# Kernel tuning notes

Hardware: AMD Instinct MI355X
Metric: run time of the kernel (lower is better)

The kernel has to match this reference:

```python
import jax, jax.numpy as jnp
import numpy as np

N = 50000        # nodes
E = 800000       # edges (before self-loops)
F_IN = 256       # n_features
HID = 32         # hidden_dims (per-head out channels)
HEADS = 4
HC = HID * HEADS # 128, per-layer width
CLASSES = 40
LAYERS = 2
SLOPE = 0.1      # negative_slope for leaky_relu in attention


def _glorot(key, shape):
    fan_in, fan_out = shape[-2], shape[-1]
    lim = np.sqrt(6.0 / (fan_in + fan_out))
    return jax.random.uniform(key, shape, jnp.float32, -lim, lim)


def setup_inputs() -> dict:
    key = jax.random.key(0)
    ks = jax.random.split(key, 7)
    x = jax.random.normal(ks[0], (N, F_IN), jnp.float32)
    edge_index = jax.random.randint(ks[1], (2, E), 0, N, jnp.int64)
    weight_in = _glorot(ks[2], (F_IN, HC))
    weight_out = _glorot(ks[3], (HC, CLASSES))
    Ws = _glorot(ks[4], (LAYERS, HC, HC))            # per-layer GATConv linear
    atts = _glorot(ks[5], (LAYERS, HEADS, 2 * HID))  # [a_src | a_dst] per head
    biases = jnp.zeros((LAYERS, HC), jnp.float32)
    return {"x": x, "edge_index": edge_index, "weight_in": weight_in,
            "Ws": Ws, "atts": atts, "biases": biases, "weight_out": weight_out}


def _gat_conv(h, src, dst, W, att, bias):
    # h: [N, HC]; src/dst: [E'] edge endpoints (message src -> dst)
    n = h.shape[0]
    hp = (h @ W).reshape(n, HEADS, HID)                       # [N, H, C]
    a_src, a_dst = att[:, :HID], att[:, HID:]                 # [H, C] each
    alpha_src = jnp.einsum('nhc,hc->nh', hp, a_src)           # [N, H]
    alpha_dst = jnp.einsum('nhc,hc->nh', hp, a_dst)
    logits = jax.nn.leaky_relu(alpha_src[src] + alpha_dst[dst], SLOPE)  # [E', H]
    # softmax over edges grouped by destination node
    m = jax.ops.segment_max(logits, dst, num_segments=n)      # [N, H]
    e = jnp.exp(logits - m[dst])
    z = jax.ops.segment_sum(e, dst, num_segments=n)           # [N, H]
    alpha = e / z[dst]                                        # [E', H]
    msg = hp[src] * alpha[:, :, None]                         # [E', H, C]
    out = jax.ops.segment_sum(msg, dst, num_segments=n)       # [N, H, C]
    return out.reshape(n, HC) + bias


def reference(x, edge_index, weight_in, Ws, atts, biases, weight_out):
    # add self-loops (PyG GATConv default)
    loop = jnp.arange(N, dtype=edge_index.dtype)
    src = jnp.concatenate([edge_index[0], loop])
    dst = jnp.concatenate([edge_index[1], loop])
    h = x @ weight_in
    for l in range(LAYERS):
        # dropout is identity in eval mode
        h = jax.nn.elu(_gat_conv(h, src, dst, Ws[l], atts[l], biases[l]))
    return jax.nn.log_softmax(h @ weight_out, axis=1)
```

## Files before the change

kernel.cpp:

```cpp
#include <hip/hip_runtime.h>
#include <hip/hip_bf16.h>
#include <math.h>

#define N_NODES 50000
#define N_EDGES 800000
#define F_IN 256
#define HID 32
#define HEADS 4
#define HC 128
#define CLASSES 40
#define LAYERS 2
#define SLOPE 0.1f
#define EE (N_EDGES + N_NODES)

#define BSHIFT 9
#define NBUCK 98
#define CHUNK 4096
#define NBLK_E ((EE + CHUNK - 1) / CHUNK)

typedef unsigned short ushortT;
typedef unsigned int uintT;
typedef __attribute__((ext_vector_type(8))) short short8v;
typedef __attribute__((ext_vector_type(4))) float f32x4;

__device__ __forceinline__ ushortT f2bu(float f) {
    __hip_bfloat16 h = __float2bfloat16(f);
    ushortT u; __builtin_memcpy(&u, &h, 2); return u;
}

__device__ __forceinline__ void scan_buckets(const int* __restrict__ bcnt,
                                             int* sbase, int t) {
    if (t < 64) {
        int i0 = 2 * t, i1 = 2 * t + 1;
        int v0 = (i0 < NBUCK) ? bcnt[i0] : 0;
        int v1 = (i1 < NBUCK) ? bcnt[i1] : 0;
        int s = v0 + v1;
        int x = s;
#pragma unroll
        for (int off = 1; off < 64; off <<= 1) {
            int y = __shfl_up(x, off);
            if (t >= off) x += y;
        }
        int excl = x - s;
        if (i0 <= NBUCK) sbase[i0] = excl;
        if (i1 <= NBUCK) sbase[i1] = excl + v0;
    }
    __syncthreads();
}

__global__ void wconv_all(const float* __restrict__ w_in, const float* __restrict__ Ws,
                          const float* __restrict__ w_out, ushortT* __restrict__ w_inT,
                          ushortT* __restrict__ WsT, ushortT* __restrict__ woutT,
                          int* __restrict__ bcnt, int* __restrict__ gcur0,
                          int* __restrict__ rowptr) {
    int i = blockIdx.x * 256 + threadIdx.x;
    if (i < NBUCK) { bcnt[i] = 0; gcur0[i] = 0; }
    if (i == NBUCK) rowptr[N_NODES] = EE;
    if (i < 32768) {
        int r = i >> 7, c = i & 127;
        w_inT[(size_t)c * F_IN + r] = f2bu(w_in[i]);
    } else if (i < 65536) {
        int j = i - 32768;
        int l = j >> 14, jj = j & 16383;
        int r = jj >> 7, c = jj & 127;
        WsT[l * 16384 + c * 128 + r] = f2bu(Ws[j]);
    } else if (i < 65536 + 6144) {
        int j = i - 65536;
        int c = j >> 7, k = j & 127;
        woutT[j] = (c < CLASSES) ? f2bu(w_out[k * CLASSES + c]) : (ushortT)0;
    }
}

#define AS_LD 40
template<bool AF32>
__global__ __launch_bounds__(256) void gemm_mfma(const void* __restrict__ Aptr,
                                                 const ushortT* __restrict__ BT,
                                                 ushortT* __restrict__ Cb,
                                                 const float* __restrict__ att,
                                                 float* __restrict__ asrc,
                                                 float* __restrict__ adst,
                                                 int M, int K) {
    __shared__ ushortT As[64 * AS_LD];
    __shared__ ushortT Bs[128 * AS_LD];
    int t = threadIdx.x;
    int w = t >> 6, lane = t & 63;
    int row0 = blockIdx.x * 64;
    int ar = t >> 2, ak = (t & 3) * 8;
    int bcol = t >> 1, bks = (t & 1) * 16;
    int wr = w * 16;
    int arow = wr + (lane & 15);
    int ak8 = (lane >> 4) * 8;
    f32x4 acc[8] = {};

    for (int k0 = 0; k0 < K; k0 += 32) {
        int grow = row0 + ar;
        if (AF32) {
            const float* A = (const float*)Aptr;
            float4 v0 = make_float4(0.f, 0.f, 0.f, 0.f), v1 = v0;
            if (grow < M) {
                const float* ap = A + (size_t)grow * K + k0 + ak;
                v0 = *(const float4*)ap;
                v1 = *(const float4*)(ap + 4);
            }
            uint4 p;
            p.x = (uintT)f2bu(v0.x) | ((uintT)f2bu(v0.y) << 16);
            p.y = (uintT)f2bu(v0.z) | ((uintT)f2bu(v0.w) << 16);
            p.z = (uintT)f2bu(v1.x) | ((uintT)f2bu(v1.y) << 16);
            p.w = (uintT)f2bu(v1.z) | ((uintT)f2bu(v1.w) << 16);
            *(uint4*)&As[ar * AS_LD + ak] = p;
        } else {
            const ushortT* A = (const ushortT*)Aptr;
            uint4 p = make_uint4(0, 0, 0, 0);
            if (grow < M) p = *(const uint4*)(A + (size_t)grow * K + k0 + ak);
            *(uint4*)&As[ar * AS_LD + ak] = p;
        }
        {
            const ushortT* bp = BT + (size_t)bcol * K + k0 + bks;
            *(uint4*)&Bs[bcol * AS_LD + bks]     = *(const uint4*)bp;
            *(uint4*)&Bs[bcol * AS_LD + bks + 8] = *(const uint4*)(bp + 8);
        }
        __syncthreads();
        short8v a = *(short8v*)&As[arow * AS_LD + ak8];
#pragma unroll
        for (int c = 0; c < 8; ++c) {
            short8v b = *(short8v*)&Bs[(c * 16 + (lane & 15)) * AS_LD + ak8];
            acc[c] = __builtin_amdgcn_mfma_f32_16x16x32_bf16(a, b, acc[c], 0, 0, 0);
        }
        __syncthreads();
    }
    int cl = lane & 15;
    int r0 = row0 + wr + ((lane >> 4) << 2);
#pragma unroll
    for (int c = 0; c < 8; ++c) {
        int cc = c * 16 + cl;
#pragma unroll
        for (int r = 0; r < 4; ++r) {
            int rr = r0 + r;
            if (rr < M) Cb[(size_t)rr * 128 + cc] = f2bu(acc[c][r]);
        }
    }
    if (att) {
#pragma unroll
        for (int h = 0; h < HEADS; ++h) {
            float as0 = att[h * 64 + cl];
            float as1 = att[h * 64 + 16 + cl];
            float ad0 = att[h * 64 + 32 + cl];
            float ad1 = att[h * 64 + 48 + cl];
#pragma unroll
            for (int r = 0; r < 4; ++r) {
                float ps = acc[2 * h][r] * as0 + acc[2 * h + 1][r] * as1;
                float pd = acc[2 * h][r] * ad0 + acc[2 * h + 1][r] * ad1;
#pragma unroll
                for (int off = 1; off < 16; off <<= 1) {
                    ps += __shfl_xor(ps, off);
                    pd += __shfl_xor(pd, off);
                }
                int rr = r0 + r;
                if (cl == 0 && rr < M) {
                    asrc[rr * 4 + h] = ps;
                    adst[rr * 4 + h] = pd;
                }
            }
        }
    }
}

__global__ __launch_bounds__(256) void cls_mfma(const ushortT* __restrict__ A,
                                                const ushortT* __restrict__ BT,
                                                float* __restrict__ out, int M) {
    __shared__ ushortT As[64 * AS_LD];
    __shared__ ushortT Bs[48 * AS_LD];
    int t = threadIdx.x;
    int w = t >> 6, lane = t & 63;
    int row0 = blockIdx.x * 64;
    int ar = t >> 2, ak = (t & 3) * 8;
    int wr = w * 16;
    int arow = wr + (lane & 15);
    int ak8 = (lane >> 4) * 8;
    f32x4 acc[3] = {};

    for (int k0 = 0; k0 < 128; k0 += 32) {
        int grow = row0 + ar;
        uint4 p = make_uint4(0, 0, 0, 0);
        if (grow < M) p = *(const uint4*)(A + (size_t)grow * 128 + k0 + ak);
        *(uint4*)&As[ar * AS_LD + ak] = p;
        if (t < 96) {
            int bcol = t >> 1, bks = (t & 1) * 16;
            const ushortT* bp = BT + bcol * 128 + k0 + bks;
            *(uint4*)&Bs[bcol * AS_LD + bks]     = *(const uint4*)bp;
            *(uint4*)&Bs[bcol * AS_LD + bks + 8] = *(const uint4*)(bp + 8);
        }
        __syncthreads();
        short8v a = *(short8v*)&As[arow * AS_LD + ak8];
#pragma unroll
        for (int c = 0; c < 3; ++c) {
            short8v b = *(short8v*)&Bs[(c * 16 + (lane & 15)) * AS_LD + ak8];
            acc[c] = __builtin_amdgcn_mfma_f32_16x16x32_bf16(a, b, acc[c], 0, 0, 0);
        }
        __syncthreads();
    }
    int cl = lane & 15;
    int r0 = row0 + wr + ((lane >> 4) << 2);
#pragma unroll
    for (int r = 0; r < 4; ++r) {
        float v0 = acc[0][r], v1 = acc[1][r];
        float v2 = (cl < 8) ? acc[2][r] : -1e30f;
        float m = fmaxf(fmaxf(v0, v1), v2);
#pragma unroll
        for (int off = 1; off < 16; off <<= 1) m = fmaxf(m, __shfl_xor(m, off));
        float e = __expf(v0 - m) + __expf(v1 - m) + ((cl < 8) ? __expf(v2 - m) : 0.f);
#pragma unroll
        for (int off = 1; off < 16; off <<= 1) e += __shfl_xor(e, off);
        float ls = m + __logf(e);
        int rr = r0 + r;
        if (rr < M) {
            float* o = out + (size_t)rr * CLASSES;
            o[cl] = v0 - ls;
            o[16 + cl] = v1 - ls;
            if (cl < 8) o[32 + cl] = v2 - ls;
        }
    }
}

__global__ __launch_bounds__(256) void bucket_count(const int* __restrict__ ei,
                                                    int* __restrict__ bcnt) {
    __shared__ int hist[NBUCK];
    int t = threadIdx.x;
    if (t < NBUCK) hist[t] = 0;
    __syncthreads();
    int base = blockIdx.x * CHUNK;
    int end = min(base + CHUNK, EE);
    for (int i = base + t; i < end; i += 256) {
        int d = (i < N_EDGES) ? ei[N_EDGES + i] : (i - N_EDGES);
        atomicAdd(&hist[d >> BSHIFT], 1);
    }
    __syncthreads();
    if (t < NBUCK && hist[t]) atomicAdd(&bcnt[t], hist[t]);
}

__global__ __launch_bounds__(256) void bucket_scatter(const int* __restrict__ ei,
                                                      const int* __restrict__ bcnt,
                                                      int* __restrict__ gcur0,
                                                      uintT* __restrict__ ebuf) {
    __shared__ int sbase[NBUCK + 2];
    __shared__ int hist[NBUCK];
    __shared__ int rbase[NBUCK];
    int t = threadIdx.x;
    scan_buckets(bcnt, sbase, t);
    if (t < NBUCK) hist[t] = 0;
    __syncthreads();
    int base = blockIdx.x * CHUNK;
    int end = min(base + CHUNK, EE);
    for (int i = base + t; i < end; i += 256) {
        int d = (i < N_EDGES) ? ei[N_EDGES + i] : (i - N_EDGES);
        atomicAdd(&hist[d >> BSHIFT], 1);
    }
    __syncthreads();
    if (t < NBUCK) {
        int c = hist[t];
        rbase[t] = c ? (sbase[t] + atomicAdd(&gcur0[t], c)) : 0;
    }
    __syncthreads();
    if (t < NBUCK) hist[t] = 0;
    __syncthreads();
    for (int i = base + t; i < end; i += 256) {
        int s, d;
        if (i < N_EDGES) { s = ei[i]; d = ei[N_EDGES + i]; } else { s = d = i - N_EDGES; }
        int b = d >> BSHIFT;
        int pos = rbase[b] + atomicAdd(&hist[b], 1);
        ebuf[pos] = ((uintT)s << BSHIFT) | (uintT)(d & 511);
    }
}

__global__ __launch_bounds__(256) void csr_local(const uintT* __restrict__ ebuf,
                                                 const int* __restrict__ bcnt,
                                                 int* __restrict__ rowptr,
                                                 int* __restrict__ ssrc) {
    __shared__ int sbase[NBUCK + 2];
    __shared__ int cnt[512];
    __shared__ int cur[512];
    __shared__ int wsum[4];
    int b = blockIdx.x;
    int t = threadIdx.x;
    scan_buckets(bcnt, sbase, t);
    int node0 = b << BSHIFT;
    int nb = min(512, N_NODES - node0);
    int beg = sbase[b], end = sbase[b + 1];
    cnt[t] = 0; cnt[t + 256] = 0;
    __syncthreads();
    for (int i = beg + t; i < end; i += 256)
        atomicAdd(&cnt[ebuf[i] & 511], 1);
    __syncthreads();
    int v0 = cnt[2 * t], v1 = cnt[2 * t + 1];
    int s = v0 + v1;
    int lane = t & 63, w = t >> 6;
    int x = s;
#pragma unroll
    for (int off = 1; off < 64; off <<= 1) { int y = __shfl_up(x, off); if (lane >= off) x += y; }
    if (lane == 63) wsum[w] = x;
    __syncthreads();
    if (t == 0) { int run = 0; for (int k = 0; k < 4; ++k) { int tmp = wsum[k]; wsum[k] = run; run += tmp; } }
    __syncthreads();
    int excl = wsum[w] + x - s;
    cnt[2 * t] = excl; cnt[2 * t + 1] = excl + v0;
    cur[2 * t] = excl; cur[2 * t + 1] = excl + v0;
    if (2 * t < nb)     rowptr[node0 + 2 * t]     = beg + excl;
    if (2 * t + 1 < nb) rowptr[node0 + 2 * t + 1] = beg + excl + v0;
    __syncthreads();
    for (int i = beg + t; i < end; i += 256) {
        uintT e = ebuf[i];
        int pos = beg + atomicAdd(&cur[e & 511], 1);
        ssrc[pos] = (int)(e >> BSHIFT);
    }
}

__device__ __forceinline__ float lrelu(float v) { return v > 0.f ? v : SLOPE * v; }

__device__ __forceinline__ void gat_one(
    int node, int beg, int deg, int lane,
    const int* __restrict__ ssrc, const float* __restrict__ asrc,
    const float* __restrict__ adst, const ushortT* __restrict__ hpb,
    const float* __restrict__ bias, ushortT* __restrict__ foutB,
    float* sexp, int* ssrcl, float* sm)
{
    float4 ad = *(const float4*)(adst + (size_t)node * 4);
    int g = lane >> 4, i0 = lane & 15;
    float acc0 = 0.f, acc1 = 0.f;
    float zinv;
    const ushortT* hrow = hpb + lane * 2;

    if (deg <= 64) {
        float4 lg = make_float4(-1e30f, -1e30f, -1e30f, -1e30f);
        int soff = 0;
        if (lane < deg) {
            int s = ssrc[beg + lane];
            float4 a = *(const float4*)(asrc + (size_t)s * 4);
            lg.x = lrelu(a.x + ad.x);
            lg.y = lrelu(a.y + ad.y);
            lg.z = lrelu(a.z + ad.z);
            lg.w = lrelu(a.w + ad.w);
            soff = s * HC;
        }
        ssrcl[lane] = soff;
        *(float4*)&sexp[lane * 4] = lg;
        asm volatile("s_waitcnt lgkmcnt(0)" ::: "memory");
        float mg =     sexp[i0 * 4 + g];
        mg = fmaxf(mg, sexp[(i0 + 16) * 4 + g]);
        mg = fmaxf(mg, sexp[(i0 + 32) * 4 + g]);
        mg = fmaxf(mg, sexp[(i0 + 48) * 4 + g]);
#pragma unroll
        for (int off = 1; off < 16; off <<= 1) mg = fmaxf(mg, __shfl_xor(mg, off));
        if (i0 == 0) sm[g] = mg;
        asm volatile("s_waitcnt lgkmcnt(0)" ::: "memory");
        float4 m = *(float4*)&sm[0];
        float4 ex;
        ex.x = __expf(lg.x - m.x);
        ex.y = __expf(lg.y - m.y);
        ex.z = __expf(lg.z - m.z);
        ex.w = __expf(lg.w - m.w);
        *(float4*)&sexp[lane * 4] = ex;
        asm volatile("s_waitcnt lgkmcnt(0)" ::: "memory");
        float zg = sexp[i0 * 4 + g];
        zg +=      sexp[(i0 + 16) * 4 + g];
        zg +=      sexp[(i0 + 32) * 4 + g];
        zg +=      sexp[(i0 + 48) * 4 + g];
#pragma unroll
        for (int off = 1; off < 16; off <<= 1) zg += __shfl_xor(zg, off);
        zinv = 1.f / zg;
#pragma unroll 4
        for (int i = 0; i < deg; ++i) {
            float e = sexp[i * 4 + g];
            int off = ssrcl[i];
            uintT u = *(const uintT*)(hrow + off);
            acc0 = fmaf(__uint_as_float(u << 16),         e, acc0);
            acc1 = fmaf(__uint_as_float(u & 0xffff0000u), e, acc1);
        }
    } else {
        float4 m = make_float4(-1e30f, -1e30f, -1e30f, -1e30f);
        for (int i = lane; i < deg; i += 64) {
            int s = ssrc[beg + i];
            float4 a = *(const float4*)(asrc + (size_t)s * 4);
            m.x = fmaxf(m.x, lrelu(a.x + ad.x));
            m.y = fmaxf(m.y, lrelu(a.y + ad.y));
            m.z = fmaxf(m.z, lrelu(a.z + ad.z));
            m.w = fmaxf(m.w, lrelu(a.w + ad.w));
        }
#pragma unroll
        for (int off = 1; off < 64; off <<= 1) {
            m.x = fmaxf(m.x, __shfl_xor(m.x, off));
            m.y = fmaxf(m.y, __shfl_xor(m.y, off));
            m.z = fmaxf(m.z, __shfl_xor(m.z, off));
            m.w = fmaxf(m.w, __shfl_xor(m.w, off));
        }
        float4 zp = make_float4(0.f, 0.f, 0.f, 0.f);
        for (int c0 = 0; c0 < deg; c0 += 64) {
            int n_ch = min(64, deg - c0);
            if (lane < n_ch) {
                int s = ssrc[beg + c0 + lane];
                float4 a = *(const float4*)(asrc + (size_t)s * 4);
                float4 ex;
                ex.x = __expf(lrelu(a.x + ad.x) - m.x);
                ex.y = __expf(lrelu(a.y + ad.y) - m.y);
                ex.z = __expf(lrelu(a.z + ad.z) - m.z);
                ex.w = __expf(lrelu(a.w + ad.w) - m.w);
                *(float4*)&sexp[lane * 4] = ex;
                ssrcl[lane] = s * HC;
                zp.x += ex.x; zp.y += ex.y; zp.z += ex.z; zp.w += ex.w;
            }
            asm volatile("s_waitcnt lgkmcnt(0)" ::: "memory");
#pragma unroll 4
            for (int i = 0; i < n_ch; ++i) {
                float e = sexp[i * 4 + g];
                int off = ssrcl[i];
                uintT u = *(const uintT*)(hrow + off);
                acc0 = fmaf(__uint_as_float(u << 16),         e, acc0);
                acc1 = fmaf(__uint_as_float(u & 0xffff0000u), e, acc1);
            }
        }
#pragma unroll
        for (int off = 1; off < 64; off <<= 1) {
            zp.x += __shfl_xor(zp.x, off);
            zp.y += __shfl_xor(zp.y, off);
            zp.z += __shfl_xor(zp.z, off);
            zp.w += __shfl_xor(zp.w, off);
        }
        float zh = (g == 0) ? zp.x : (g == 1) ? zp.y : (g == 2) ? zp.z : zp.w;
        zinv = 1.f / zh;
    }

    float b0 = bias[lane * 2], b1 = bias[lane * 2 + 1];
    float v0 = acc0 * zinv + b0; v0 = v0 > 0.f ? v0 : __expf(v0) - 1.f;
    float v1 = acc1 * zinv + b1; v1 = v1 > 0.f ? v1 : __expf(v1) - 1.f;
    *(uintT*)(foutB + (size_t)node * HC + lane * 2) =
        (uintT)f2bu(v0) | ((uintT)f2bu(v1) << 16);
}

#define WPB 4
__global__ __launch_bounds__(256) void gat_gather2(
    const int* __restrict__ rowptr, const int* __restrict__ ssrc,
    const float* __restrict__ asrc, const float* __restrict__ adst,
    const ushortT* __restrict__ hpb, const float* __restrict__ bias,
    ushortT* __restrict__ foutB)
{
    __shared__ __align__(16) float s_exp[WPB][64][4];
    __shared__ int   s_src[WPB][64];
    __shared__ __align__(16) float s_m[WPB][8];
    __shared__ __align__(16) float s_z[WPB][8];
    int w = threadIdx.x >> 6;
    int lane = threadIdx.x & 63;
    int widx = blockIdx.x * WPB + w;
    int n0 = widx * 2;
    if (n0 >= N_NODES) return;
    int beg0 = rowptr[n0];
    int mid  = rowptr[n0 + 1];
    int end1 = rowptr[n0 + 2];
    int deg0 = mid - beg0, deg1 = end1 - mid;

    if (deg0 <= 32 && deg1 <= 32) {
        int half = lane >> 5;
        int ll = lane & 31;
        int nn = n0 + half;
        int mybeg = half ? mid : beg0;
        int mydeg = half ? deg1 : deg0;
        float4 ad = *(const float4*)(adst + (size_t)nn * 4);
        float4 lg = make_float4(-1e30f, -1e30f, -1e30f, -1e30f);
        int soff = 0;
        if (ll < mydeg) {
            int s = ssrc[mybeg + ll];
            float4 a = *(const float4*)(asrc + (size_t)s * 4);
            lg.x = lrelu(a.x + ad.x);
            lg.y = lrelu(a.y + ad.y);
            lg.z = lrelu(a.z + ad.z);
            lg.w = lrelu(a.w + ad.w);
            soff = s * HC;
        }
        s_src[w][lane] = soff;
        *(float4*)&s_exp[w][lane][0] = lg;
        asm volatile("s_waitcnt lgkmcnt(0)" ::: "memory");
        int grp = lane >> 3, gi = lane & 7;
        int gbase = (grp >> 2) << 5;
        int gh = grp & 3;
        float mg =     s_exp[w][gbase + gi][gh];
        mg = fmaxf(mg, s_exp[w][gbase + gi +  8][gh]);
        mg = fmaxf(mg, s_exp[w][gbase + gi + 16][gh]);
        mg = fmaxf(mg, s_exp[w][gbase + gi + 24][gh]);
        mg = fmaxf(mg, __shfl_xor(mg, 1));
        mg = fmaxf(mg, __shfl_xor(mg, 2));
        mg = fmaxf(mg, __shfl_xor(mg, 4));
        if (gi == 0) s_m[w][grp] = mg;
        asm volatile("s_waitcnt lgkmcnt(0)" ::: "memory");
        float4 m = *(float4*)&s_m[w][half * 4];
        float4 ex;
        ex.x = __expf(lg.x - m.x);
        ex.y = __expf(lg.y - m.y);
        ex.z = __expf(lg.z - m.z);
        ex.w = __expf(lg.w - m.w);
        *(float4*)&s_exp[w][lane][0] = ex;
        asm volatile("s_waitcnt lgkmcnt(0)" ::: "memory");
        float zg = s_exp[w][gbase + gi][gh];
        zg +=      s_exp[w][gbase + gi +  8][gh];
        zg +=      s_exp[w][gbase + gi + 16][gh];
        zg +=      s_exp[w][gbase + gi + 24][gh];
        zg += __shfl_xor(zg, 1);
        zg += __shfl_xor(zg, 2);
        zg += __shfl_xor(zg, 4);
        if (gi == 0) s_z[w][grp] = zg;
        asm volatile("s_waitcnt lgkmcnt(0)" ::: "memory");
        int hd = ll >> 3;
        float zinv = 1.f / s_z[w][half * 4 + hd];
        int maxdeg = max(deg0, deg1);
        int ebase = half << 5;
        const ushortT* hrow = hpb + ll * 4;
        float a0 = 0.f, a1 = 0.f, a2 = 0.f, a3 = 0.f;
#pragma unroll 4
        for (int i = 0; i < maxdeg; ++i) {
            float e = s_exp[w][ebase + i][hd];
            int off = s_src[w][ebase + i];
            uint2 u = *(const uint2*)(hrow + off);
            a0 = fmaf(__uint_as_float(u.x << 16),         e, a0);
            a1 = fmaf(__uint_as_float(u.x & 0xffff0000u), e, a1);
            a2 = fmaf(__uint_as_float(u.y << 16),         e, a2);
            a3 = fmaf(__uint_as_float(u.y & 0xffff0000u), e, a3);
        }
        const float* bp = bias + ll * 4;
        float v0 = a0 * zinv + bp[0]; v0 = v0 > 0.f ? v0 : __expf(v0) - 1.f;
        float v1 = a1 * zinv + bp[1]; v1 = v1 > 0.f ? v1 : __expf(v1) - 1.f;
        float v2 = a2 * zinv + bp[2]; v2 = v2 > 0.f ? v2 : __expf(v2) - 1.f;
        float v3 = a3 * zinv + bp[3]; v3 = v3 > 0.f ? v3 : __expf(v3) - 1.f;
        uint2 o;
        o.x = (uintT)f2bu(v0) | ((uintT)f2bu(v1) << 16);
        o.y = (uintT)f2bu(v2) | ((uintT)f2bu(v3) << 16);
        *(uint2*)(foutB + (size_t)nn * HC + ll * 4) = o;
    } else {
        gat_one(n0,     beg0, deg0, lane, ssrc, asrc, adst, hpb, bias, foutB,
                &s_exp[w][0][0], &s_src[w][0], &s_m[w][0]);
        gat_one(n0 + 1, mid,  deg1, lane, ssrc, asrc, adst, hpb, bias, foutB,
                &s_exp[w][0][0], &s_src[w][0], &s_m[w][0]);
    }
}

extern "C" void kernel_launch(void* const* d_in, const int* in_sizes, int n_in,
                              void* d_out, int out_size, void* d_ws, size_t ws_size,
                              hipStream_t stream) {
    const float* x      = (const float*)d_in[0];
    const int*   ei     = (const int*)d_in[1];
    const float* w_in   = (const float*)d_in[2];
    const float* Ws     = (const float*)d_in[3];
    const float* atts   = (const float*)d_in[4];
    const float* biases = (const float*)d_in[5];
    const float* w_out  = (const float*)d_in[6];
    float* out = (float*)d_out;

    char* wp = (char*)d_ws;
    ushortT* hb0 = (ushortT*)wp; wp += (size_t)N_NODES * HC * 2;
    ushortT* hb1 = (ushortT*)wp; wp += (size_t)N_NODES * HC * 2;
    ushortT* hpb = (ushortT*)wp; wp += (size_t)N_NODES * HC * 2;
    float* asrc  = (float*)wp;   wp += (size_t)N_NODES * HEADS * 4;
    float* adst  = (float*)wp;   wp += (size_t)N_NODES * HEADS * 4;
    int* rowptr  = (int*)wp;     wp += (size_t)(N_NODES + 4) * 4;
    int* ssrc    = (int*)wp;     wp += (size_t)EE * 4;
    uintT* ebuf  = (uintT*)wp;   wp += (size_t)EE * 4;
    int* bcnt    = (int*)wp;     wp += (size_t)(NBUCK + 4) * 4;
    int* gcur0   = (int*)wp;     wp += (size_t)(NBUCK + 4) * 4;
    ushortT* w_inT = (ushortT*)wp; wp += (size_t)HC * F_IN * 2;
    ushortT* WsT   = (ushortT*)wp; wp += (size_t)LAYERS * HC * HC * 2;
    ushortT* woutT = (ushortT*)wp; wp += (size_t)48 * HC * 2;

    wconv_all<<<(32768 + 32768 + 6144 + 255) / 256, 256, 0, stream>>>(
        w_in, Ws, w_out, w_inT, WsT, woutT, bcnt, gcur0, rowptr);

    bucket_count<<<NBLK_E, 256, 0, stream>>>(ei, bcnt);
    bucket_scatter<<<NBLK_E, 256, 0, stream>>>(ei, bcnt, gcur0, ebuf);
    csr_local<<<NBUCK, 256, 0, stream>>>(ebuf, bcnt, rowptr, ssrc);

    int gblk = (N_NODES + 63) / 64;
    gemm_mfma<true><<<gblk, 256, 0, stream>>>(x, w_inT, hb0, nullptr, nullptr, nullptr,
                                              N_NODES, F_IN);

    const ushortT* hin_b = hb0;
    ushortT* gout[LAYERS] = { hb1, hb0 };
    int g2blk = (N_NODES / 2 + WPB - 1) / WPB;
    for (int l = 0; l < LAYERS; ++l) {
        gemm_mfma<false><<<gblk, 256, 0, stream>>>(hin_b, WsT + (size_t)l * HC * HC, hpb,
                                                   atts + (size_t)l * HEADS * 2 * HID,
                                                   asrc, adst, N_NODES, HC);
        gat_gather2<<<g2blk, 64 * WPB, 0, stream>>>(
            rowptr, ssrc, asrc, adst, hpb, biases + (size_t)l * HC, gout[l]);
        hin_b = gout[l];
    }

    cls_mfma<<<gblk, 256, 0, stream>>>(hb0, woutT, out, N_NODES);
}
```

Baseline: 182.1 us.

## Merge independent graph-preprocessing kernels into GEMM launches via block-range dispatch

```diff
diff --git a/kernel.cpp b/kernel.cpp
--- a/kernel.cpp
+++ b/kernel.cpp
@@ -17,6 +17,7 @@
 #define NBUCK 98
 #define CHUNK 4096
 #define NBLK_E ((EE + CHUNK - 1) / CHUNK)
+#define GEMM_BLOCKS ((N_NODES + 63) / 64)
 
 typedef unsigned short ushortT;
 typedef unsigned int uintT;
@@ -73,18 +74,17 @@
 
 #define AS_LD 40
 template<bool AF32>
-__global__ __launch_bounds__(256) void gemm_mfma(const void* __restrict__ Aptr,
-                                                 const ushortT* __restrict__ BT,
-                                                 ushortT* __restrict__ Cb,
-                                                 const float* __restrict__ att,
-                                                 float* __restrict__ asrc,
-                                                 float* __restrict__ adst,
-                                                 int M, int K) {
-    __shared__ ushortT As[64 * AS_LD];
-    __shared__ ushortT Bs[128 * AS_LD];
+__device__ __forceinline__ void gemm_body(ushortT* As, ushortT* Bs,
+                                          const void* __restrict__ Aptr,
+                                          const ushortT* __restrict__ BT,
+                                          ushortT* __restrict__ Cb,
+                                          const float* __restrict__ att,
+                                          float* __restrict__ asrc,
+                                          float* __restrict__ adst,
+                                          int M, int K, int bid) {
     int t = threadIdx.x;
     int w = t >> 6, lane = t & 63;
-    int row0 = blockIdx.x * 64;
+    int row0 = bid * 64;
     int ar = t >> 2, ak = (t & 3) * 8;
     int bcol = t >> 1, bks = (t & 1) * 16;
     int wr = w * 16;
@@ -165,6 +165,143 @@
     }
 }
 
+template<bool AF32>
+__global__ __launch_bounds__(256) void gemm_mfma(const void* __restrict__ Aptr,
+                                                 const ushortT* __restrict__ BT,
+                                                 ushortT* __restrict__ Cb,
+                                                 const float* __restrict__ att,
+                                                 float* __restrict__ asrc,
+                                                 float* __restrict__ adst,
+                                                 int M, int K) {
+    __shared__ ushortT As[64 * AS_LD];
+    __shared__ ushortT Bs[128 * AS_LD];
+    gemm_body<AF32>(As, Bs, Aptr, BT, Cb, att, asrc, adst, M, K, blockIdx.x);
+}
+
+__device__ __forceinline__ void csr_local_body(const uintT* __restrict__ ebuf,
+                                               const int* __restrict__ bcnt,
+                                               int* __restrict__ rowptr,
+                                               int* __restrict__ ssrc, int b,
+                                               int* sbase, int* cnt, int* cur,
+                                               int* wsum) {
+    int t = threadIdx.x;
+    scan_buckets(bcnt, sbase, t);
+    int node0 = b << BSHIFT;
+    int nb = min(512, N_NODES - node0);
+    int beg = sbase[b], end = sbase[b + 1];
+    cnt[t] = 0; cnt[t + 256] = 0;
+    __syncthreads();
+    for (int i = beg + t; i < end; i += 256)
+        atomicAdd(&cnt[ebuf[i] & 511], 1);
+    __syncthreads();
+    int v0 = cnt[2 * t], v1 = cnt[2 * t + 1];
+    int s = v0 + v1;
+    int lane = t & 63, w = t >> 6;
+    int x = s;
+#pragma unroll
+    for (int off = 1; off < 64; off <<= 1) { int y = __shfl_up(x, off); if (lane >= off) x += y; }
+    if (lane == 63) wsum[w] = x;
+    __syncthreads();
+    if (t == 0) { int run = 0; for (int k = 0; k < 4; ++k) { int tmp = wsum[k]; wsum[k] = run; run += tmp; } }
+    __syncthreads();
+    int excl = wsum[w] + x - s;
+    cnt[2 * t] = excl; cnt[2 * t + 1] = excl + v0;
+    cur[2 * t] = excl; cur[2 * t + 1] = excl + v0;
+    if (2 * t < nb)     rowptr[node0 + 2 * t]     = beg + excl;
+    if (2 * t + 1 < nb) rowptr[node0 + 2 * t + 1] = beg + excl + v0;
+    __syncthreads();
+    for (int i = beg + t; i < end; i += 256) {
+        uintT e = ebuf[i];
+        int pos = beg + atomicAdd(&cur[e & 511], 1);
+        ssrc[pos] = (int)(e >> BSHIFT);
+    }
+}
+
+__global__ __launch_bounds__(256) void gemm0_count(const float* __restrict__ x,
+                                                   const ushortT* __restrict__ w_inT,
+                                                   ushortT* __restrict__ hb0,
+                                                   const int* __restrict__ ei,
+                                                   int* __restrict__ bcnt) {
+    __shared__ ushortT As[64 * AS_LD];
+    __shared__ ushortT Bs[128 * AS_LD];
+    __shared__ int hist[NBUCK];
+    if (blockIdx.x < GEMM_BLOCKS) {
+        gemm_body<true>(As, Bs, x, w_inT, hb0, nullptr, nullptr, nullptr,
+                        N_NODES, F_IN, blockIdx.x);
+    } else {
+        int t = threadIdx.x;
+        if (t < NBUCK) hist[t] = 0;
+        __syncthreads();
+        int base = (blockIdx.x - GEMM_BLOCKS) * CHUNK;
+        int end = min(base + CHUNK, EE);
+        for (int i = base + t; i < end; i += 256) {
+            int d = (i < N_EDGES) ? ei[N_EDGES + i] : (i - N_EDGES);
+            atomicAdd(&hist[d >> BSHIFT], 1);
+        }
+        __syncthreads();
+        if (t < NBUCK && hist[t]) atomicAdd(&bcnt[t], hist[t]);
+    }
+}
+
+__global__ __launch_bounds__(256) void gemm_csr(const ushortT* __restrict__ hin,
+                                                const ushortT* __restrict__ BT,
+                                                ushortT* __restrict__ hpb,
+                                                const float* __restrict__ att,
+                                                float* __restrict__ asrc,
+                                                float* __restrict__ adst,
+                                                const uintT* __restrict__ ebuf,
+                                                const int* __restrict__ bcnt,
+                                                int* __restrict__ rowptr,
+                                                int* __restrict__ ssrc) {
+    __shared__ ushortT As[64 * AS_LD];
+    __shared__ ushortT Bs[128 * AS_LD];
+    __shared__ int sbase[NBUCK + 2];
+    __shared__ int cnt[512];
+    __shared__ int cur[512];
+    __shared__ int wsum[4];
+    if (blockIdx.x < GEMM_BLOCKS) {
+        gemm_body<false>(As, Bs, hin, BT, hpb, att, asrc, adst,
+                         N_NODES, HC, blockIdx.x);
+    } else {
+        csr_local_body(ebuf, bcnt, rowptr, ssrc, blockIdx.x - GEMM_BLOCKS,
+                       sbase, cnt, cur, wsum);
+    }
+}
+
+__global__ __launch_bounds__(256) void bucket_scatter(const int* __restrict__ ei,
+                                                      const int* __restrict__ bcnt,
+                                                      int* __restrict__ gcur0,
+                                                      uintT* __restrict__ ebuf) {
+    __shared__ int sbase[NBUCK + 2];
+    __shared__ int hist[NBUCK];
+    __shared__ int rbase[NBUCK];
+    int t = threadIdx.x;
+    scan_buckets(bcnt, sbase, t);
+    if (t < NBUCK) hist[t] = 0;
+    __syncthreads();
+    int base = blockIdx.x * CHUNK;
+    int end = min(base + CHUNK, EE);
+    for (int i = base + t; i < end; i += 256) {
+        int d = (i < N_EDGES) ? ei[N_EDGES + i] : (i - N_EDGES);
+        atomicAdd(&hist[d >> BSHIFT], 1);
+    }
+    __syncthreads();
+    if (t < NBUCK) {
+        int c = hist[t];
+        rbase[t] = c ? (sbase[t] + atomicAdd(&gcur0[t], c)) : 0;
+    }
+    __syncthreads();
+    if (t < NBUCK) hist[t] = 0;
+    __syncthreads();
+    for (int i = base + t; i < end; i += 256) {
+        int s, d;
+        if (i < N_EDGES) { s = ei[i]; d = ei[N_EDGES + i]; } else { s = d = i - N_EDGES; }
+        int b = d >> BSHIFT;
+        int pos = rbase[b] + atomicAdd(&hist[b], 1);
+        ebuf[pos] = ((uintT)s << BSHIFT) | (uintT)(d & 511);
+    }
+}
+
 __global__ __launch_bounds__(256) void cls_mfma(const ushortT* __restrict__ A,
                                                 const ushortT* __restrict__ BT,
                                                 float* __restrict__ out, int M) {
@@ -219,98 +356,6 @@
             o[16 + cl] = v1 - ls;
             if (cl < 8) o[32 + cl] = v2 - ls;
         }
-    }
-}
-
-__global__ __launch_bounds__(256) void bucket_count(const int* __restrict__ ei,
-                                                    int* __restrict__ bcnt) {
-    __shared__ int hist[NBUCK];
-    int t = threadIdx.x;
-    if (t < NBUCK) hist[t] = 0;
-    __syncthreads();
-    int base = blockIdx.x * CHUNK;
-    int end = min(base + CHUNK, EE);
-    for (int i = base + t; i < end; i += 256) {
-        int d = (i < N_EDGES) ? ei[N_EDGES + i] : (i - N_EDGES);
-        atomicAdd(&hist[d >> BSHIFT], 1);
-    }
-    __syncthreads();
-    if (t < NBUCK && hist[t]) atomicAdd(&bcnt[t], hist[t]);
-}
-
-__global__ __launch_bounds__(256) void bucket_scatter(const int* __restrict__ ei,
-                                                      const int* __restrict__ bcnt,
-                                                      int* __restrict__ gcur0,
-                                                      uintT* __restrict__ ebuf) {
-    __shared__ int sbase[NBUCK + 2];
-    __shared__ int hist[NBUCK];
-    __shared__ int rbase[NBUCK];
-    int t = threadIdx.x;
-    scan_buckets(bcnt, sbase, t);
-    if (t < NBUCK) hist[t] = 0;
-    __syncthreads();
-    int base = blockIdx.x * CHUNK;
-    int end = min(base + CHUNK, EE);
-    for (int i = base + t; i < end; i += 256) {
-        int d = (i < N_EDGES) ? ei[N_EDGES + i] : (i - N_EDGES);
-        atomicAdd(&hist[d >> BSHIFT], 1);
-    }
-    __syncthreads();
-    if (t < NBUCK) {
-        int c = hist[t];
-        rbase[t] = c ? (sbase[t] + atomicAdd(&gcur0[t], c)) : 0;
-    }
-    __syncthreads();
-    if (t < NBUCK) hist[t] = 0;
-    __syncthreads();
-    for (int i = base + t; i < end; i += 256) {
-        int s, d;
-        if (i < N_EDGES) { s = ei[i]; d = ei[N_EDGES + i]; } else { s = d = i - N_EDGES; }
-        int b = d >> BSHIFT;
-        int pos = rbase[b] + atomicAdd(&hist[b], 1);
-        ebuf[pos] = ((uintT)s << BSHIFT) | (uintT)(d & 511);
-    }
-}
-
-__global__ __launch_bounds__(256) void csr_local(const uintT* __restrict__ ebuf,
-                                                 const int* __restrict__ bcnt,
-                                                 int* __restrict__ rowptr,
-                                                 int* __restrict__ ssrc) {
-    __shared__ int sbase[NBUCK + 2];
-    __shared__ int cnt[512];
-    __shared__ int cur[512];
-    __shared__ int wsum[4];
-    int b = blockIdx.x;
-    int t = threadIdx.x;
-    scan_buckets(bcnt, sbase, t);
-    int node0 = b << BSHIFT;
-    int nb = min(512, N_NODES - node0);
-    int beg = sbase[b], end = sbase[b + 1];
-    cnt[t] = 0; cnt[t + 256] = 0;
-    __syncthreads();
-    for (int i = beg + t; i < end; i += 256)
-        atomicAdd(&cnt[ebuf[i] & 511], 1);
-    __syncthreads();
-    int v0 = cnt[2 * t], v1 = cnt[2 * t + 1];
-    int s = v0 + v1;
-    int lane = t & 63, w = t >> 6;
-    int x = s;
-#pragma unroll
-    for (int off = 1; off < 64; off <<= 1) { int y = __shfl_up(x, off); if (lane >= off) x += y; }
-    if (lane == 63) wsum[w] = x;
-    __syncthreads();
-    if (t == 0) { int run = 0; for (int k = 0; k < 4; ++k) { int tmp = wsum[k]; wsum[k] = run; run += tmp; } }
-    __syncthreads();
-    int excl = wsum[w] + x - s;
-    cnt[2 * t] = excl; cnt[2 * t + 1] = excl + v0;
-    cur[2 * t] = excl; cur[2 * t + 1] = excl + v0;
-    if (2 * t < nb)     rowptr[node0 + 2 * t]     = beg + excl;
-    if (2 * t + 1 < nb) rowptr[node0 + 2 * t + 1] = beg + excl + v0;
-    __syncthreads();
-    for (int i = beg + t; i < end; i += 256) {
-        uintT e = ebuf[i];
-        int pos = beg + atomicAdd(&cur[e & 511], 1);
-        ssrc[pos] = (int)(e >> BSHIFT);
     }
 }
 
@@ -569,25 +614,22 @@
     wconv_all<<<(32768 + 32768 + 6144 + 255) / 256, 256, 0, stream>>>(
         w_in, Ws, w_out, w_inT, WsT, woutT, bcnt, gcur0, rowptr);
 
-    bucket_count<<<NBLK_E, 256, 0, stream>>>(ei, bcnt);
+    gemm0_count<<<GEMM_BLOCKS + NBLK_E, 256, 0, stream>>>(x, w_inT, hb0, ei, bcnt);
+
     bucket_scatter<<<NBLK_E, 256, 0, stream>>>(ei, bcnt, gcur0, ebuf);
-    csr_local<<<NBUCK, 256, 0, stream>>>(ebuf, bcnt, rowptr, ssrc);
-
-    int gblk = (N_NODES + 63) / 64;
-    gemm_mfma<true><<<gblk, 256, 0, stream>>>(x, w_inT, hb0, nullptr, nullptr, nullptr,
-                                              N_NODES, F_IN);
-
-    const ushortT* hin_b = hb0;
-    ushortT* gout[LAYERS] = { hb1, hb0 };
+
+    gemm_csr<<<GEMM_BLOCKS + NBUCK, 256, 0, stream>>>(
+        hb0, WsT, hpb, atts, asrc, adst, ebuf, bcnt, rowptr, ssrc);
+
     int g2blk = (N_NODES / 2 + WPB - 1) / WPB;
-    for (int l = 0; l < LAYERS; ++l) {
-        gemm_mfma<false><<<gblk, 256, 0, stream>>>(hin_b, WsT + (size_t)l * HC * HC, hpb,
-                                                   atts + (size_t)l * HEADS * 2 * HID,
-                                                   asrc, adst, N_NODES, HC);
-        gat_gather2<<<g2blk, 64 * WPB, 0, stream>>>(
-            rowptr, ssrc, asrc, adst, hpb, biases + (size_t)l * HC, gout[l]);
-        hin_b = gout[l];
-    }
-
-    cls_mfma<<<gblk, 256, 0, stream>>>(hb0, woutT, out, N_NODES);
-}
+    gat_gather2<<<g2blk, 64 * WPB, 0, stream>>>(
+        rowptr, ssrc, asrc, adst, hpb, biases, hb1);
+
+    gemm_mfma<false><<<GEMM_BLOCKS, 256, 0, stream>>>(
+        hb1, WsT + (size_t)HC * HC, hpb, atts + (size_t)HEADS * 2 * HID,
+        asrc, adst, N_NODES, HC);
+    gat_gather2<<<g2blk, 64 * WPB, 0, stream>>>(
+        rowptr, ssrc, asrc, adst, hpb, biases + HC, hb0);
+
+    cls_mfma<<<GEMM_BLOCKS, 256, 0, stream>>>(hb0, woutT, out, N_NODES);
+}
```

Result: faster. 165.9 us (-8.9%).
